# Optimization experiments

Measured on AMD Instinct MI355X. Metric: run time of the kernel, lower is better.

## Reference

```python
import jax, jax.numpy as jnp
import numpy as np

STRIDE = 2  # ksize = [1, STRIDE, 1, 1]: unpool along height only
B, H, W, C = 8, 512, 256, 64


def setup_inputs() -> dict:
    key = jax.random.key(0)
    k1, k2 = jax.random.split(key)
    inputs = jax.random.normal(k1, (B, H, W, C), dtype=jnp.float32)
    # TF argmax-style flat indices into the per-batch output grid [2H, W, C]
    mask = jax.random.randint(k2, (B, H, W, C), 0, STRIDE * H * W * C, dtype=jnp.int64)
    return {"inputs": inputs, "mask": mask}


def reference(inputs, mask):
    b_, h, w, c = inputs.shape
    out_h = h * STRIDE  # output_shape = (B, stride*H, W, C)
    # Decode flat per-batch indices exactly as the TF layer does
    y = mask // (w * c)
    x = (mask % (w * c)) // c
    b = jnp.arange(b_, dtype=jnp.int64)[:, None, None, None]  # batch_range
    f = jnp.arange(c, dtype=jnp.int64)                        # feature_range
    # tf.scatter_nd sums duplicate indices; .at[].add matches that semantics
    out = jnp.zeros((b_, out_h, w, c), dtype=inputs.dtype)
    out = out.at[b, y, x, f].add(inputs)
    return out
```

## Files before the change

kernel.cpp:

```cpp
#include <hip/hip_runtime.h>


typedef unsigned int u32;
typedef unsigned short u16;
typedef unsigned long long u64;

typedef int   iv4 __attribute__((ext_vector_type(4)));
typedef float fv4 __attribute__((ext_vector_type(4)));

constexpr long long N_IN = 1LL << 26;
constexpr int SBS   = 8192;
constexpr int NSB   = (int)(N_IN / SBS);
constexpr int NBKT  = 512;
constexpr int NWIN  = 4096;
constexpr int RSH   = 15;
constexpr int RSLOTS = 1 << RSH;
constexpr int SB_PER_B = 1024;

constexpr size_t OFF_RECA = 0;
constexpr size_t OFF_DIR  = (size_t)N_IN * 8;
constexpr size_t OFF_DIRT = OFF_DIR + (size_t)NSB * NBKT * 2;
constexpr size_t WS_FUSED = OFF_DIRT + (size_t)NWIN * SB_PER_B * 2;

__global__ __launch_bounds__(512) void passA(const float* __restrict__ in,
                                             const int* __restrict__ mask,
                                             u64* __restrict__ recA,
                                             u16* __restrict__ dir)
{
    __shared__ u32 cur[NBKT];
    __shared__ u32 wsum[8];
    __shared__ u64 sRec[SBS];
    const int tid = threadIdx.x;
    const int sb  = blockIdx.x;
    const int e0  = sb * SBS + tid * 16;

    const iv4* m4 = (const iv4*)mask + (e0 >> 2);
    const fv4* v4 = (const fv4*)in + (e0 >> 2);
    iv4 m0 = __builtin_nontemporal_load(m4 + 0);
    iv4 m1 = __builtin_nontemporal_load(m4 + 1);
    iv4 m2 = __builtin_nontemporal_load(m4 + 2);
    iv4 m3 = __builtin_nontemporal_load(m4 + 3);
    fv4 va = __builtin_nontemporal_load(v4 + 0);
    fv4 vb = __builtin_nontemporal_load(v4 + 1);
    fv4 vc = __builtin_nontemporal_load(v4 + 2);
    fv4 vd = __builtin_nontemporal_load(v4 + 3);
    const u32 bbits = ((u32)(e0 >> 23)) << 24;
    const u32 c0 = (u32)(e0 & 63);

    u32 tg[16]; float vv[16];
    tg[ 0] = bbits + (((u32)m0.x) & ~63u) + c0 +  0; vv[ 0] = va.x;
    tg[ 1] = bbits + (((u32)m0.y) & ~63u) + c0 +  1; vv[ 1] = va.y;
    tg[ 2] = bbits + (((u32)m0.z) & ~63u) + c0 +  2; vv[ 2] = va.z;
    tg[ 3] = bbits + (((u32)m0.w) & ~63u) + c0 +  3; vv[ 3] = va.w;
    tg[ 4] = bbits + (((u32)m1.x) & ~63u) + c0 +  4; vv[ 4] = vb.x;
    tg[ 5] = bbits + (((u32)m1.y) & ~63u) + c0 +  5; vv[ 5] = vb.y;
    tg[ 6] = bbits + (((u32)m1.z) & ~63u) + c0 +  6; vv[ 6] = vb.z;
    tg[ 7] = bbits + (((u32)m1.w) & ~63u) + c0 +  7; vv[ 7] = vb.w;
    tg[ 8] = bbits + (((u32)m2.x) & ~63u) + c0 +  8; vv[ 8] = vc.x;
    tg[ 9] = bbits + (((u32)m2.y) & ~63u) + c0 +  9; vv[ 9] = vc.y;
    tg[10] = bbits + (((u32)m2.z) & ~63u) + c0 + 10; vv[10] = vc.z;
    tg[11] = bbits + (((u32)m2.w) & ~63u) + c0 + 11; vv[11] = vc.w;
    tg[12] = bbits + (((u32)m3.x) & ~63u) + c0 + 12; vv[12] = vd.x;
    tg[13] = bbits + (((u32)m3.y) & ~63u) + c0 + 13; vv[13] = vd.y;
    tg[14] = bbits + (((u32)m3.z) & ~63u) + c0 + 14; vv[14] = vd.z;
    tg[15] = bbits + (((u32)m3.w) & ~63u) + c0 + 15; vv[15] = vd.w;

    cur[tid] = 0;
    __syncthreads();
#pragma unroll
    for (int j = 0; j < 16; ++j) atomicAdd(&cur[(tg[j] >> RSH) & (NBKT - 1)], 1u);
    __syncthreads();

    {
        const int lane = tid & 63;
        const int wid  = tid >> 6;
        u32 x = cur[tid];
        u32 s = x;
#pragma unroll
        for (int d = 1; d < 64; d <<= 1) {
            u32 n = __shfl_up(s, (unsigned)d, 64);
            if (lane >= d) s += n;
        }
        if (lane == 63) wsum[wid] = s;
        u32 exw = s - x;
        __syncthreads();
        if (tid == 0) {
            u32 run = 0;
#pragma unroll
            for (int w = 0; w < 8; ++w) { u32 t2 = wsum[w]; wsum[w] = run; run += t2; }
        }
        __syncthreads();
        u32 start = wsum[wid] + exw;
        dir[(size_t)sb * NBKT + tid] = (u16)start;
        cur[tid] = start;
    }
    __syncthreads();

#pragma unroll
    for (int j = 0; j < 16; ++j) {
        u32 p = atomicAdd(&cur[(tg[j] >> RSH) & (NBKT - 1)], 1u);
        sRec[p] = ((u64)(tg[j] & (RSLOTS - 1)) << 32) | (u64)__float_as_uint(vv[j]);
    }
    __syncthreads();
#pragma unroll
    for (int k = 0; k < 16; ++k) {
        int i = tid + k * 512;
        recA[(size_t)sb * SBS + i] = sRec[i];
    }
}

__global__ __launch_bounds__(256) void tposeD(const u16* __restrict__ dir,
                                              u16* __restrict__ dirT)
{
    __shared__ u16 t[64][65];
    const int tx = threadIdx.x;
    const int ty = threadIdx.y;
    const int bb = blockIdx.z;
    const int sb0 = blockIdx.x * 64;
    const int lb0 = blockIdx.y * 64;
#pragma unroll
    for (int k = 0; k < 16; ++k) {
        int row = k * 4 + ty;
        t[row][tx] = dir[((size_t)(bb * SB_PER_B + sb0 + row)) * NBKT + lb0 + tx];
    }
    __syncthreads();
#pragma unroll
    for (int k = 0; k < 16; ++k) {
        int row = k * 4 + ty;
        dirT[((size_t)(bb * NBKT + lb0 + row)) * SB_PER_B + sb0 + tx] = t[tx][row];
    }
}

__global__ __launch_bounds__(1024) void passC(const u64* __restrict__ recA,
                                              const u16* __restrict__ dirT,
                                              float* __restrict__ out)
{
    __shared__ float acc[RSLOTS];
    __shared__ u32 cSrc[SB_PER_B];
    __shared__ u16 cLen[SB_PER_B];
    const int tid = threadIdx.x;
    const int bid = blockIdx.x;
    const int w   = ((bid & 7) << 9) | (bid >> 3);
    const int bb  = w >> 9;
    const int lb  = w & (NBKT - 1);

    {
        u32 st = dirT[(size_t)w * SB_PER_B + tid];
        u32 en = (lb == NBKT - 1) ? (u32)SBS : (u32)dirT[(size_t)(w + 1) * SB_PER_B + tid];
        cSrc[tid] = (u32)(bb * SB_PER_B + tid) * (u32)SBS + st;
        cLen[tid] = (u16)(en - st);
    }
    for (int i = tid; i < RSLOTS; i += 1024) acc[i] = 0.f;
    __syncthreads();

    const int g  = tid >> 4;
    const int gl = tid & 15;
    for (int s2 = g; s2 < SB_PER_B; s2 += 128) {
        const int s3 = s2 + 64;
        u32 srcA = cSrc[s2];  int lenA = (int)cLen[s2];
        u32 srcB = cSrc[s3];  int lenB = (int)cLen[s3];
        u64 a0 = 0, a1 = 0, b0 = 0, b1 = 0;
        const bool pa0 = gl < lenA, pa1 = gl + 16 < lenA;
        const bool pb0 = gl < lenB, pb1 = gl + 16 < lenB;
        if (pa0) a0 = recA[srcA + gl];
        if (pa1) a1 = recA[srcA + gl + 16];
        if (pb0) b0 = recA[srcB + gl];
        if (pb1) b1 = recA[srcB + gl + 16];
        if (pa0) atomicAdd(&acc[(u32)(a0 >> 32)], __uint_as_float((u32)a0));
        if (pa1) atomicAdd(&acc[(u32)(a1 >> 32)], __uint_as_float((u32)a1));
        if (pb0) atomicAdd(&acc[(u32)(b0 >> 32)], __uint_as_float((u32)b0));
        if (pb1) atomicAdd(&acc[(u32)(b1 >> 32)], __uint_as_float((u32)b1));
        for (int off = gl + 32; off < lenA; off += 16) {
            u64 rec = recA[srcA + off];
            atomicAdd(&acc[(u32)(rec >> 32)], __uint_as_float((u32)rec));
        }
        for (int off = gl + 32; off < lenB; off += 16) {
            u64 rec = recA[srcB + off];
            atomicAdd(&acc[(u32)(rec >> 32)], __uint_as_float((u32)rec));
        }
    }
    __syncthreads();

    fv4* o4 = (fv4*)out + ((size_t)w << (RSH - 2));
    const fv4* a4 = (const fv4*)acc;
#pragma unroll
    for (int i = tid; i < RSLOTS / 4; i += 1024)
        __builtin_nontemporal_store(a4[i], o4 + i);
}

__global__ __launch_bounds__(256) void unmaxpool_scatter(
    const float* __restrict__ in, const int* __restrict__ mask,
    float* __restrict__ out)
{
    const long long n4 = N_IN / 4;
    long long gidx = (long long)blockIdx.x * blockDim.x + threadIdx.x;
    const long long stride = (long long)gridDim.x * blockDim.x;
    for (; gidx < n4; gidx += stride) {
        float4 v = reinterpret_cast<const float4*>(in)[gidx];
        int4 m = reinterpret_cast<const int4*>(mask)[gidx];
        long long i0 = gidx * 4;
        u32 ob = ((u32)(i0 >> 23)) << 24;
        u32 c0 = (u32)(i0 & 63);
        atomicAdd(&out[ob + (u32)(m.x & ~63) + c0 + 0], v.x);
        atomicAdd(&out[ob + (u32)(m.y & ~63) + c0 + 1], v.y);
        atomicAdd(&out[ob + (u32)(m.z & ~63) + c0 + 2], v.z);
        atomicAdd(&out[ob + (u32)(m.w & ~63) + c0 + 3], v.w);
    }
}

extern "C" void kernel_launch(void* const* d_in, const int* in_sizes, int n_in,
                              void* d_out, int out_size, void* d_ws, size_t ws_size,
                              hipStream_t stream) {
    const float* in = (const float*)d_in[0];
    const int* mask = (const int*)d_in[1];
    float* out = (float*)d_out;
    char* ws = (char*)d_ws;

    if (d_ws != nullptr && ws_size >= WS_FUSED) {
        u64* recA = (u64*)(ws + OFF_RECA);
        u16* dir  = (u16*)(ws + OFF_DIR);
        u16* dirT = (u16*)(ws + OFF_DIRT);
        passA<<<NSB, 512, 0, stream>>>(in, mask, recA, dir);
        tposeD<<<dim3(16, 8, 8), dim3(64, 4), 0, stream>>>(dir, dirT);
        passC<<<NWIN, 1024, 0, stream>>>(recA, dirT, out);
    } else {
        (void)hipMemsetAsync(out, 0, (size_t)out_size * sizeof(float), stream);
        unmaxpool_scatter<<<2048, 256, 0, stream>>>(in, mask, out);
    }
}
```

Baseline: 673.4 us.

## Halve passC accumulation window to 16K slots with 1024 buckets

Doubles the radix buckets per superblock (1024 instead of 512) so each passC block accumulates a 16K-float window instead of 32K. This halves the LDS footprint per block so more 1024-thread blocks can fit per CU, aiming to hide gather latency. Pass A's scan now handles two buckets per thread, and the transpose grid grows to match. passC is reworked to process four source segments per group with one initial record each, because segments are now shorter. The directory arrays double in size, so the required workspace grows; if it exceeds ws_size, the slow atomic fallback is used instead.

```diff
diff --git a/kernel.cpp b/kernel.cpp
--- a/kernel.cpp
+++ b/kernel.cpp
@@ -11,9 +11,9 @@
 constexpr long long N_IN = 1LL << 26;
 constexpr int SBS   = 8192;
 constexpr int NSB   = (int)(N_IN / SBS);
-constexpr int NBKT  = 512;
-constexpr int NWIN  = 4096;
-constexpr int RSH   = 15;
+constexpr int NBKT  = 1024;
+constexpr int NWIN  = 8192;
+constexpr int RSH   = 14;
 constexpr int RSLOTS = 1 << RSH;
 constexpr int SB_PER_B = 1024;
 
@@ -65,7 +65,8 @@
     tg[14] = bbits + (((u32)m3.z) & ~63u) + c0 + 14; vv[14] = vd.z;
     tg[15] = bbits + (((u32)m3.w) & ~63u) + c0 + 15; vv[15] = vd.w;
 
-    cur[tid] = 0;
+    cur[2 * tid] = 0;
+    cur[2 * tid + 1] = 0;
     __syncthreads();
 #pragma unroll
     for (int j = 0; j < 16; ++j) atomicAdd(&cur[(tg[j] >> RSH) & (NBKT - 1)], 1u);
@@ -74,15 +75,17 @@
     {
         const int lane = tid & 63;
         const int wid  = tid >> 6;
-        u32 x = cur[tid];
-        u32 s = x;
+        u32 a = cur[2 * tid];
+        u32 b = cur[2 * tid + 1];
+        u32 sum = a + b;
+        u32 s = sum;
 #pragma unroll
         for (int d = 1; d < 64; d <<= 1) {
             u32 n = __shfl_up(s, (unsigned)d, 64);
             if (lane >= d) s += n;
         }
         if (lane == 63) wsum[wid] = s;
-        u32 exw = s - x;
+        u32 exw = s - sum;
         __syncthreads();
         if (tid == 0) {
             u32 run = 0;
@@ -91,8 +94,10 @@
         }
         __syncthreads();
         u32 start = wsum[wid] + exw;
-        dir[(size_t)sb * NBKT + tid] = (u16)start;
-        cur[tid] = start;
+        dir[(size_t)sb * NBKT + 2 * tid]     = (u16)start;
+        dir[(size_t)sb * NBKT + 2 * tid + 1] = (u16)(start + a);
+        cur[2 * tid]     = start;
+        cur[2 * tid + 1] = start + a;
     }
     __syncthreads();
 
@@ -131,17 +136,17 @@
     }
 }
 
-__global__ __launch_bounds__(1024) void passC(const u64* __restrict__ recA,
-                                              const u16* __restrict__ dirT,
-                                              float* __restrict__ out)
+__global__ __launch_bounds__(1024, 8) void passC(const u64* __restrict__ recA,
+                                                 const u16* __restrict__ dirT,
+                                                 float* __restrict__ out)
 {
     __shared__ float acc[RSLOTS];
     __shared__ u32 cSrc[SB_PER_B];
     __shared__ u16 cLen[SB_PER_B];
     const int tid = threadIdx.x;
     const int bid = blockIdx.x;
-    const int w   = ((bid & 7) << 9) | (bid >> 3);
-    const int bb  = w >> 9;
+    const int w   = ((bid & 7) << 10) | (bid >> 3);
+    const int bb  = w >> 10;
     const int lb  = w & (NBKT - 1);
 
     {
@@ -155,27 +160,39 @@
 
     const int g  = tid >> 4;
     const int gl = tid & 15;
-    for (int s2 = g; s2 < SB_PER_B; s2 += 128) {
-        const int s3 = s2 + 64;
-        u32 srcA = cSrc[s2];  int lenA = (int)cLen[s2];
-        u32 srcB = cSrc[s3];  int lenB = (int)cLen[s3];
-        u64 a0 = 0, a1 = 0, b0 = 0, b1 = 0;
-        const bool pa0 = gl < lenA, pa1 = gl + 16 < lenA;
-        const bool pb0 = gl < lenB, pb1 = gl + 16 < lenB;
-        if (pa0) a0 = recA[srcA + gl];
-        if (pa1) a1 = recA[srcA + gl + 16];
-        if (pb0) b0 = recA[srcB + gl];
-        if (pb1) b1 = recA[srcB + gl + 16];
-        if (pa0) atomicAdd(&acc[(u32)(a0 >> 32)], __uint_as_float((u32)a0));
-        if (pa1) atomicAdd(&acc[(u32)(a1 >> 32)], __uint_as_float((u32)a1));
-        if (pb0) atomicAdd(&acc[(u32)(b0 >> 32)], __uint_as_float((u32)b0));
-        if (pb1) atomicAdd(&acc[(u32)(b1 >> 32)], __uint_as_float((u32)b1));
-        for (int off = gl + 32; off < lenA; off += 16) {
+    for (int s0 = g; s0 < SB_PER_B; s0 += 256) {
+        const int s1 = s0 + 64, s2 = s0 + 128, s3 = s0 + 192;
+        u32 srcA = cSrc[s0];  int lenA = (int)cLen[s0];
+        u32 srcB = cSrc[s1];  int lenB = (int)cLen[s1];
+        u32 srcC = cSrc[s2];  int lenC = (int)cLen[s2];
+        u32 srcD = cSrc[s3];  int lenD = (int)cLen[s3];
+        u64 a0 = 0, b0 = 0, c0 = 0, d0 = 0;
+        const bool pa = gl < lenA;
+        const bool pb = gl < lenB;
+        const bool pc = gl < lenC;
+        const bool pd = gl < lenD;
+        if (pa) a0 = recA[srcA + gl];
+        if (pb) b0 = recA[srcB + gl];
+        if (pc) c0 = recA[srcC + gl];
+        if (pd) d0 = recA[srcD + gl];
+        if (pa) atomicAdd(&acc[(u32)(a0 >> 32)], __uint_as_float((u32)a0));
+        if (pb) atomicAdd(&acc[(u32)(b0 >> 32)], __uint_as_float((u32)b0));
+        if (pc) atomicAdd(&acc[(u32)(c0 >> 32)], __uint_as_float((u32)c0));
+        if (pd) atomicAdd(&acc[(u32)(d0 >> 32)], __uint_as_float((u32)d0));
+        for (int off = gl + 16; off < lenA; off += 16) {
             u64 rec = recA[srcA + off];
             atomicAdd(&acc[(u32)(rec >> 32)], __uint_as_float((u32)rec));
         }
-        for (int off = gl + 32; off < lenB; off += 16) {
+        for (int off = gl + 16; off < lenB; off += 16) {
             u64 rec = recA[srcB + off];
+            atomicAdd(&acc[(u32)(rec >> 32)], __uint_as_float((u32)rec));
+        }
+        for (int off = gl + 16; off < lenC; off += 16) {
+            u64 rec = recA[srcC + off];
+            atomicAdd(&acc[(u32)(rec >> 32)], __uint_as_float((u32)rec));
+        }
+        for (int off = gl + 16; off < lenD; off += 16) {
+            u64 rec = recA[srcD + off];
             atomicAdd(&acc[(u32)(rec >> 32)], __uint_as_float((u32)rec));
         }
     }
@@ -221,7 +238,7 @@
         u16* dir  = (u16*)(ws + OFF_DIR);
         u16* dirT = (u16*)(ws + OFF_DIRT);
         passA<<<NSB, 512, 0, stream>>>(in, mask, recA, dir);
-        tposeD<<<dim3(16, 8, 8), dim3(64, 4), 0, stream>>>(dir, dirT);
+        tposeD<<<dim3(16, 16, 8), dim3(64, 4), 0, stream>>>(dir, dirT);
         passC<<<NWIN, 1024, 0, stream>>>(recA, dirT, out);
     } else {
         (void)hipMemsetAsync(out, 0, (size_t)out_size * sizeof(float), stream);
```

After: 620.1 us. 7.9% less time.
